# Optimization experiments

Hardware: AMD Instinct MI355X
Metric: run time of the kernel (lower is better)

## Reference

```python
import jax, jax.numpy as jnp
import numpy as np

D_EMB = 256
SCALE = 0.02
B, T = 4, 4096
EPS = 1e-5


def layer_norm(x, w, b):
    m = jnp.mean(x, axis=-1, keepdims=True)
    v = jnp.mean((x - m) ** 2, axis=-1, keepdims=True)
    return (x - m) * jax.lax.rsqrt(v + EPS) * w + b


def setup_inputs() -> dict:
    key = jax.random.key(0)
    ks = jax.random.split(key, 4)
    x = jax.random.normal(ks[0], (B, T, D_EMB), dtype=jnp.float32)
    qkv = jax.random.normal(ks[1], (3, D_EMB, D_EMB), dtype=jnp.float32) * SCALE
    # nn.Linear(D, 2D, bias=False): weight shape (2D, D), applied as x @ W.T
    w1 = jax.random.normal(ks[2], (2 * D_EMB, D_EMB), dtype=jnp.float32) * (1.0 / np.sqrt(D_EMB))
    w2 = jax.random.normal(ks[3], (D_EMB, 2 * D_EMB), dtype=jnp.float32) * (1.0 / np.sqrt(2 * D_EMB))
    ones = jnp.ones((D_EMB,), dtype=jnp.float32)
    zeros = jnp.zeros((D_EMB,), dtype=jnp.float32)
    return {
        "x": x, "qkv": qkv,
        "ln_q_w": ones, "ln_q_b": zeros,
        "ln_k_w": ones, "ln_k_b": zeros,
        "ln_attn_w": ones, "ln_attn_b": zeros,
        "w1": w1, "w2": w2,
        "ln_ff_w": ones, "ln_ff_b": zeros,
    }


def reference(x, qkv, ln_q_w, ln_q_b, ln_k_w, ln_k_b, ln_attn_w, ln_attn_b, w1, w2, ln_ff_w, ln_ff_b):
    # QKV projections: [3, B, T, D]
    y = jnp.einsum('btd,ndD->nbtD', x, qkv)
    q, k, v = y[0], y[1], y[2]
    q = layer_norm(q, ln_q_w, ln_q_b)
    k = layer_norm(k, ln_k_w, ln_k_b)
    # full (non-causal) single-head attention, scale by sqrt(D_EMB)
    scores = jnp.einsum('btd,bsd->bts', q, k) / jnp.sqrt(jnp.float32(D_EMB))
    attn = jax.nn.softmax(scores, axis=-1)
    y = jnp.einsum('bts,bsd->btd', attn, v)
    y = layer_norm(y, ln_attn_w, ln_attn_b)
    x = 0.7 * (x + y)
    # FFN with dual leaky_relu
    y = jax.nn.leaky_relu(x @ w1.T, negative_slope=0.2)
    y = jax.nn.leaky_relu(y @ w2.T, negative_slope=0.2)
    y = layer_norm(y, ln_ff_w, ln_ff_b)
    return 0.7 * (x + y)
```

## Files before the change

kernel.cpp:

```cpp
#include <hip/hip_runtime.h>

#define BSZ   4
#define TSEQ  4096
#define DEMB  256
#define NTOK  (BSZ * TSEQ)
#define HID   512
#define SPLITS 4
#define KEYS_PER_SPLIT (TSEQ / SPLITS)
#define TK 32
#define KIMG_STRIDE 8704
#define VIMG_STRIDE 10240

using bf16x8 = __attribute__((ext_vector_type(8))) short;
using f32x16 = __attribute__((ext_vector_type(16))) float;

static __device__ __forceinline__ unsigned short f2bf(float f) {
  union { float f; unsigned u; } v; v.f = f;
  unsigned r = v.u + 0x7FFF + ((v.u >> 16) & 1);
  return (unsigned short)(r >> 16);
}
static __device__ __forceinline__ float bf2f(unsigned short u) {
  union { unsigned u; float f; } v; v.u = ((unsigned)u) << 16;
  return v.f;
}

static __device__ __forceinline__ void async16(void* lds, const void* gp) {
  __builtin_amdgcn_global_load_lds(
      (const __attribute__((address_space(1))) unsigned int*)gp,
      (__attribute__((address_space(3))) unsigned int*)lds, 16, 0, 0);
}

__global__ __launch_bounds__(256) void prep_kernel(
    const float* __restrict__ qkv, const float* __restrict__ w1,
    const float* __restrict__ w2, unsigned short* __restrict__ qkvT,
    unsigned short* __restrict__ w1b, unsigned short* __restrict__ w2b)
{
  const int tid = threadIdx.x;
  if (blockIdx.y < 3) {
    if (blockIdx.x >= 16) return;
    __shared__ float Ts[64][65];
    const int z  = blockIdx.y;
    const int k0 = (blockIdx.x >> 2) * 64;
    const int j0 = (blockIdx.x & 3) * 64;
    const float* src = qkv + (size_t)z * DEMB * DEMB + (size_t)k0 * DEMB + j0;
#pragma unroll
    for (int p = 0; p < 4; ++p) {
      int idx = p * 256 + tid;
      int r = idx >> 4, g = idx & 15;
      float4 v = *(const float4*)(src + (size_t)r * DEMB + g * 4);
      Ts[r][g * 4 + 0] = v.x; Ts[r][g * 4 + 1] = v.y;
      Ts[r][g * 4 + 2] = v.z; Ts[r][g * 4 + 3] = v.w;
    }
    __syncthreads();
    unsigned short* dst = qkvT + (size_t)z * DEMB * DEMB + (size_t)j0 * DEMB + k0;
#pragma unroll
    for (int p = 0; p < 4; ++p) {
      int idx = p * 256 + tid;
      int r = idx >> 4, g = idx & 15;
      ushort4 o;
      o.x = f2bf(Ts[g * 4 + 0][r]); o.y = f2bf(Ts[g * 4 + 1][r]);
      o.z = f2bf(Ts[g * 4 + 2][r]); o.w = f2bf(Ts[g * 4 + 3][r]);
      *(ushort4*)(dst + (size_t)r * DEMB + g * 4) = o;
    }
  } else {
    const float* s = (blockIdx.y == 3) ? w1 : w2;
    unsigned short* d = (blockIdx.y == 3) ? w1b : w2b;
    const int i = blockIdx.x * 256 + tid;
    float4 v = ((const float4*)s)[i];
    ushort4 o;
    o.x = f2bf(v.x); o.y = f2bf(v.y); o.z = f2bf(v.z); o.w = f2bf(v.w);
    ((ushort4*)d)[i] = o;
  }
}

template <int ACT, int MODE, int AF32>
__global__ __launch_bounds__(256, 3) void gemm_bf16_kernel(
    const void* __restrict__ Av, const unsigned short* __restrict__ Bt,
    float* __restrict__ Cf, unsigned short* __restrict__ C0,
    unsigned short* __restrict__ C1, unsigned short* __restrict__ C2,
    int M, int N, int K)
{
  __shared__ __align__(16) unsigned short As[128 * 72];
  __shared__ __align__(16) unsigned short Bs[128 * 72];

  const int tid = threadIdx.x;
  const int w   = tid >> 6;
  const int wm  = w >> 1, wn = w & 1;
  const int l   = tid & 63;
  const int lm  = l & 31;
  const int lh  = l >> 5;

  const int m0    = blockIdx.x * 128;
  const int nbase = blockIdx.y * 128;

  f32x16 acc00, acc01, acc10, acc11;
#pragma unroll
  for (int r = 0; r < 16; ++r) { acc00[r] = 0.f; acc01[r] = 0.f; acc10[r] = 0.f; acc11[r] = 0.f; }

  const int lr = tid >> 3;
  const int lc = (tid & 7) * 8;
  const int fr = tid >> 4;
  const int fc = (tid & 15) * 4;

  const unsigned short* Ab = (const unsigned short*)Av;
  const float* Af = (const float*)Av;

  bf16x8 arb[4], brb[4];
  float4 arf[8];

#pragma unroll
  for (int i = 0; i < (AF32 ? 8 : 4); ++i) {
    if (AF32) arf[i] = *(const float4*)(Af + (size_t)(m0 + i * 16 + fr) * K + fc);
    else      arb[i] = *(const bf16x8*)(Ab + (size_t)(m0 + i * 32 + lr) * K + lc);
  }
#pragma unroll
  for (int i = 0; i < 4; ++i)
    brb[i] = *(const bf16x8*)(Bt + (size_t)(nbase + i * 32 + lr) * K + lc);

  for (int k0 = 0; k0 < K; k0 += 64) {
    __syncthreads();
    if (AF32) {
#pragma unroll
      for (int i = 0; i < 8; ++i) {
        ushort4 u;
        u.x = f2bf(arf[i].x); u.y = f2bf(arf[i].y);
        u.z = f2bf(arf[i].z); u.w = f2bf(arf[i].w);
        *(ushort4*)&As[(i * 16 + fr) * 72 + fc] = u;
      }
    } else {
#pragma unroll
      for (int i = 0; i < 4; ++i) *(bf16x8*)&As[(i * 32 + lr) * 72 + lc] = arb[i];
    }
#pragma unroll
    for (int i = 0; i < 4; ++i) *(bf16x8*)&Bs[(i * 32 + lr) * 72 + lc] = brb[i];
    __syncthreads();

    if (k0 + 64 < K) {
      const int kn = k0 + 64;
#pragma unroll
      for (int i = 0; i < (AF32 ? 8 : 4); ++i) {
        if (AF32) arf[i] = *(const float4*)(Af + (size_t)(m0 + i * 16 + fr) * K + kn + fc);
        else      arb[i] = *(const bf16x8*)(Ab + (size_t)(m0 + i * 32 + lr) * K + kn + lc);
      }
#pragma unroll
      for (int i = 0; i < 4; ++i)
        brb[i] = *(const bf16x8*)(Bt + (size_t)(nbase + i * 32 + lr) * K + kn + lc);
    }

#pragma unroll
    for (int ks = 0; ks < 4; ++ks) {
      bf16x8 a0 = *(const bf16x8*)&As[(wm * 64 + lm)      * 72 + ks * 16 + lh * 8];
      bf16x8 a1 = *(const bf16x8*)&As[(wm * 64 + 32 + lm) * 72 + ks * 16 + lh * 8];
      bf16x8 b0 = *(const bf16x8*)&Bs[(wn * 64 + lm)      * 72 + ks * 16 + lh * 8];
      bf16x8 b1 = *(const bf16x8*)&Bs[(wn * 64 + 32 + lm) * 72 + ks * 16 + lh * 8];
      acc00 = __builtin_amdgcn_mfma_f32_32x32x16_bf16(a0, b0, acc00, 0, 0, 0);
      acc01 = __builtin_amdgcn_mfma_f32_32x32x16_bf16(a0, b1, acc01, 0, 0, 0);
      acc10 = __builtin_amdgcn_mfma_f32_32x32x16_bf16(a1, b0, acc10, 0, 0, 0);
      acc11 = __builtin_amdgcn_mfma_f32_32x32x16_bf16(a1, b1, acc11, 0, 0, 0);
    }
  }

  unsigned short* Cb = C0;
  int col0, ldc;
  if (MODE == 2) {
    const int sel = blockIdx.y >> 1;
    Cb = (sel == 0) ? C0 : (sel == 1 ? C1 : C2);
    col0 = (blockIdx.y & 1) * 128;
    ldc = DEMB;
  } else {
    col0 = nbase;
    ldc = N;
  }
  const f32x16* accs[4] = { &acc00, &acc01, &acc10, &acc11 };
#pragma unroll
  for (int am = 0; am < 2; ++am)
#pragma unroll
    for (int bn = 0; bn < 2; ++bn) {
      const f32x16& a = *accs[am * 2 + bn];
#pragma unroll
      for (int r = 0; r < 16; ++r) {
        const int m = m0 + wm * 64 + am * 32 + (r & 3) + 8 * (r >> 2) + 4 * lh;
        const int n = col0 + wn * 64 + bn * 32 + lm;
        float v = a[r];
        if (ACT == 1) v = v > 0.f ? v : 0.2f * v;
        if (MODE == 0) Cf[(size_t)m * ldc + n] = v;
        else           Cb[(size_t)m * ldc + n] = f2bf(v);
      }
    }
}

__global__ __launch_bounds__(256) void ln_qk_kernel(
    const unsigned short* __restrict__ Qraw, const unsigned short* __restrict__ Kraw,
    const float* __restrict__ qw, const float* __restrict__ qb,
    const float* __restrict__ kw, const float* __restrict__ kb,
    unsigned short* __restrict__ Qbn, unsigned short* __restrict__ Kimg)
{
  const int isK = blockIdx.y;
  const unsigned short* X = isK ? Kraw : Qraw;
  const float* w = isK ? kw : qw;
  const float* b = isK ? kb : qb;
  const int lane = threadIdx.x & 63;
  const size_t row = (size_t)blockIdx.x * 4 + (threadIdx.x >> 6);
  ushort4 u = *(const ushort4*)&X[row * DEMB + lane * 4];
  float x0 = bf2f(u.x), x1 = bf2f(u.y), x2 = bf2f(u.z), x3 = bf2f(u.w);
  float s  = x0 + x1 + x2 + x3;
  float sq = x0 * x0 + x1 * x1 + x2 * x2 + x3 * x3;
#pragma unroll
  for (int o = 32; o > 0; o >>= 1) { s += __shfl_down(s, o); sq += __shfl_down(sq, o); }
  s = __shfl(s, 0); sq = __shfl(sq, 0);
  const float m  = s * (1.f / DEMB);
  const float rs = rsqrtf(sq * (1.f / DEMB) - m * m + 1e-5f);
  const float4 wv = *(const float4*)&w[lane * 4];
  const float4 bv = *(const float4*)&b[lane * 4];
  ushort4 o;
  o.x = f2bf((x0 - m) * rs * wv.x + bv.x);
  o.y = f2bf((x1 - m) * rs * wv.y + bv.y);
  o.z = f2bf((x2 - m) * rs * wv.z + bv.z);
  o.w = f2bf((x3 - m) * rs * wv.w + bv.w);
  if (!isK) {
    *(ushort4*)&Qbn[row * DEMB + lane * 4] = o;
  } else {
    const int bb = (int)(row >> 12);
    const int t  = (int)(row & 4095);
    *(ushort4*)&Kimg[(size_t)(bb * 128 + (t >> 5)) * KIMG_STRIDE + (t & 31) * 264 + lane * 4] = o;
  }
}

__global__ __launch_bounds__(256) void ln_res_kernel(
    const float* __restrict__ Y, const float* __restrict__ Xin,
    const float* __restrict__ w, const float* __restrict__ b,
    float* __restrict__ Out)
{
  const int lane = threadIdx.x & 63;
  const size_t row = (size_t)blockIdx.x * 4 + (threadIdx.x >> 6);
  float4 y = *(const float4*)&Y[row * DEMB + lane * 4];
  float s  = y.x + y.y + y.z + y.w;
  float sq = y.x * y.x + y.y * y.y + y.z * y.z + y.w * y.w;
#pragma unroll
  for (int o = 32; o > 0; o >>= 1) { s += __shfl_down(s, o); sq += __shfl_down(sq, o); }
  s = __shfl(s, 0); sq = __shfl(sq, 0);
  const float m  = s * (1.f / DEMB);
  const float rs = rsqrtf(sq * (1.f / DEMB) - m * m + 1e-5f);
  const float4 wv = *(const float4*)&w[lane * 4];
  const float4 bv = *(const float4*)&b[lane * 4];
  const float4 xi = *(const float4*)&Xin[row * DEMB + lane * 4];
  float4 o;
  o.x = 0.7f * (xi.x + (y.x - m) * rs * wv.x + bv.x);
  o.y = 0.7f * (xi.y + (y.y - m) * rs * wv.y + bv.y);
  o.z = 0.7f * (xi.z + (y.z - m) * rs * wv.z + bv.z);
  o.w = 0.7f * (xi.w + (y.w - m) * rs * wv.w + bv.w);
  *(float4*)&Out[row * DEMB + lane * 4] = o;
}

__global__ __launch_bounds__(256) void vtrans_img_kernel(
    const unsigned short* __restrict__ Vraw, unsigned short* __restrict__ Vimg)
{
  __shared__ float Ts[64][65];
  const int tid = threadIdx.x;
  const int t0 = blockIdx.x * 64;
  const int d0 = blockIdx.y * 64;
  const int b  = blockIdx.z;
  const unsigned short* src = Vraw + ((size_t)b * TSEQ + t0) * DEMB + d0;
#pragma unroll
  for (int p = 0; p < 4; ++p) {
    int idx = p * 256 + tid;
    int r = idx >> 4, g = idx & 15;
    ushort4 u = *(const ushort4*)(src + (size_t)r * DEMB + g * 4);
    Ts[r][g * 4 + 0] = bf2f(u.x); Ts[r][g * 4 + 1] = bf2f(u.y);
    Ts[r][g * 4 + 2] = bf2f(u.z); Ts[r][g * 4 + 3] = bf2f(u.w);
  }
  __syncthreads();
#pragma unroll
  for (int p = 0; p < 4; ++p) {
    int idx = p * 256 + tid;
    int r = idx >> 4, g = idx & 15;
    const int t  = t0 + g * 4;
    const int kt = t >> 5, toff = t & 31;
    ushort4 o;
    o.x = f2bf(Ts[g * 4 + 0][r]); o.y = f2bf(Ts[g * 4 + 1][r]);
    o.z = f2bf(Ts[g * 4 + 2][r]); o.w = f2bf(Ts[g * 4 + 3][r]);
    *(ushort4*)(Vimg + (size_t)(b * 128 + kt) * VIMG_STRIDE + (d0 + r) * 40 + toff) = o;
  }
}

__global__ __launch_bounds__(512) void attn_split_kernel(
    const unsigned short* __restrict__ Qb, const unsigned short* __restrict__ Kimg,
    const unsigned short* __restrict__ Vimg, unsigned short* __restrict__ Opart,
    float* __restrict__ lpart)
{
  __shared__ __align__(16) unsigned short Ks[2][KIMG_STRIDE];
  __shared__ __align__(16) unsigned short Vs[2][VIMG_STRIDE];
  __shared__ __align__(16) unsigned short Pb[8 * 32 * 40];

  const int tid = threadIdx.x;
  const int w   = tid >> 6;
  const int l   = tid & 63;
  const int lm  = l & 31;
  const int lh  = l >> 5;

  const int lin = blockIdx.x;
  const int xcd = lin & 7;
  const int idx = lin >> 3;
  const int b     = xcd >> 1;
  const int split = (xcd & 1) * 2 + (idx & 1);
  const int q0    = (idx >> 1) * 256;

  const unsigned short* Qbase  = Qb + (size_t)b * TSEQ * DEMB;
  const unsigned short* Ktiles = Kimg + (size_t)(b * 128 + split * 32) * KIMG_STRIDE;
  const unsigned short* Vtiles = Vimg + (size_t)(b * 128 + split * 32) * VIMG_STRIDE;

  bf16x8 qf[16];
  {
    const unsigned short* qrow = Qbase + (size_t)(q0 + w * 32 + lm) * DEMB + lh * 8;
#pragma unroll
    for (int ks = 0; ks < 16; ++ks) qf[ks] = *(const bf16x8*)(qrow + ks * 16);
  }

  f32x16 o[8];
  float lsum[16];
#pragma unroll
  for (int t = 0; t < 8; ++t)
#pragma unroll
    for (int r = 0; r < 16; ++r) o[t][r] = 0.f;
#pragma unroll
  for (int r = 0; r < 16; ++r) lsum[r] = 0.f;

  unsigned short* Pw = &Pb[w * 32 * 40];

#pragma unroll
  for (int i = 0; i < 3; ++i) {
    const int c = w + 8 * i;
    if (c < 17) async16(&Ks[0][c * 512], Ktiles + c * 512 + l * 8);
  }
#pragma unroll
  for (int i = 0; i < 3; ++i) {
    const int c = w + 8 * i;
    if (c < 20) async16(&Vs[0][c * 512], Vtiles + c * 512 + l * 8);
  }

  for (int st = 0; st < KEYS_PER_SPLIT / TK; ++st) {
    const int p = st & 1;
    __syncthreads();

    if (st + 1 < KEYS_PER_SPLIT / TK) {
      const unsigned short* kn = Ktiles + (size_t)(st + 1) * KIMG_STRIDE;
      const unsigned short* vn = Vtiles + (size_t)(st + 1) * VIMG_STRIDE;
#pragma unroll
      for (int i = 0; i < 3; ++i) {
        const int c = w + 8 * i;
        if (c < 17) async16(&Ks[1 - p][c * 512], kn + c * 512 + l * 8);
      }
#pragma unroll
      for (int i = 0; i < 3; ++i) {
        const int c = w + 8 * i;
        if (c < 20) async16(&Vs[1 - p][c * 512], vn + c * 512 + l * 8);
      }
    }

    f32x16 sa, sb;
#pragma unroll
    for (int r = 0; r < 16; ++r) { sa[r] = 0.f; sb[r] = 0.f; }
#pragma unroll
    for (int ks = 0; ks < 8; ++ks) {
      bf16x8 kfa = *(const bf16x8*)&Ks[p][lm * 264 + (2 * ks)     * 16 + lh * 8];
      bf16x8 kfb = *(const bf16x8*)&Ks[p][lm * 264 + (2 * ks + 1) * 16 + lh * 8];
      sa = __builtin_amdgcn_mfma_f32_32x32x16_bf16(qf[2 * ks],     kfa, sa, 0, 0, 0);
      sb = __builtin_amdgcn_mfma_f32_32x32x16_bf16(qf[2 * ks + 1], kfb, sb, 0, 0, 0);
    }

#pragma unroll
    for (int r = 0; r < 16; ++r) {
      const float pv = exp2f((sa[r] + sb[r]) * 0.09016844335f - 11.541560327f);
      lsum[r] += pv;
      const int row = (r & 3) + ((r >> 2) << 3) + (lh << 2);
      Pw[row * 40 + lm] = f2bf(pv);
    }

#pragma unroll
    for (int ks = 0; ks < 2; ++ks) {
      bf16x8 pf = *(const bf16x8*)&Pw[lm * 40 + ks * 16 + lh * 8];
#pragma unroll
      for (int t = 0; t < 8; ++t) {
        bf16x8 vf = *(const bf16x8*)&Vs[p][(t * 32 + lm) * 40 + ks * 16 + lh * 8];
        o[t] = __builtin_amdgcn_mfma_f32_32x32x16_bf16(pf, vf, o[t], 0, 0, 0);
      }
    }
  }

#pragma unroll
  for (int r = 0; r < 16; ++r) {
#pragma unroll
    for (int d = 1; d < 32; d <<= 1) lsum[r] += __shfl_xor(lsum[r], d, 64);
  }
  unsigned short* Ob =
      Opart + ((size_t)split * NTOK + (size_t)b * TSEQ + q0 + w * 32) * DEMB;
  float* lb = lpart + (size_t)split * NTOK + (size_t)b * TSEQ + q0 + w * 32;
#pragma unroll
  for (int r = 0; r < 16; ++r) {
    const int row = (r & 3) + ((r >> 2) << 3) + (lh << 2);
#pragma unroll
    for (int t = 0; t < 8; ++t)
      Ob[(size_t)row * DEMB + t * 32 + lm] = f2bf(o[t][r]);
    if (lm == 0) lb[row] = lsum[r];
  }
}

__global__ __launch_bounds__(256) void combine_lnres_kernel(
    const unsigned short* __restrict__ Opart, const float* __restrict__ lpart,
    const float* __restrict__ Xin, const float* __restrict__ w,
    const float* __restrict__ b, float* __restrict__ Out,
    unsigned short* __restrict__ Outb)
{
  const int lane = threadIdx.x & 63;
  const size_t row = (size_t)blockIdx.x * 4 + (threadIdx.x >> 6);
  float4 acc = make_float4(0.f, 0.f, 0.f, 0.f);
  float lt = 0.f;
#pragma unroll
  for (int p = 0; p < SPLITS; ++p) {
    const ushort4 u = *(const ushort4*)&Opart[((size_t)p * NTOK + row) * DEMB + lane * 4];
    acc.x += bf2f(u.x); acc.y += bf2f(u.y);
    acc.z += bf2f(u.z); acc.w += bf2f(u.w);
    lt += lpart[(size_t)p * NTOK + row];
  }
  const float inv = 1.f / lt;
  const float y0 = acc.x * inv, y1 = acc.y * inv, y2 = acc.z * inv, y3 = acc.w * inv;
  float s  = y0 + y1 + y2 + y3;
  float sq = y0 * y0 + y1 * y1 + y2 * y2 + y3 * y3;
#pragma unroll
  for (int o = 32; o > 0; o >>= 1) { s += __shfl_down(s, o); sq += __shfl_down(sq, o); }
  s = __shfl(s, 0); sq = __shfl(sq, 0);
  const float m  = s * (1.f / DEMB);
  const float rs = rsqrtf(sq * (1.f / DEMB) - m * m + 1e-5f);
  const float4 wv = *(const float4*)&w[lane * 4];
  const float4 bv = *(const float4*)&b[lane * 4];
  const float4 xi = *(const float4*)&Xin[row * DEMB + lane * 4];
  float4 o;
  o.x = 0.7f * (xi.x + (y0 - m) * rs * wv.x + bv.x);
  o.y = 0.7f * (xi.y + (y1 - m) * rs * wv.y + bv.y);
  o.z = 0.7f * (xi.z + (y2 - m) * rs * wv.z + bv.z);
  o.w = 0.7f * (xi.w + (y3 - m) * rs * wv.w + bv.w);
  *(float4*)&Out[row * DEMB + lane * 4] = o;
  ushort4 ob;
  ob.x = f2bf(o.x); ob.y = f2bf(o.y); ob.z = f2bf(o.z); ob.w = f2bf(o.w);
  *(ushort4*)&Outb[row * DEMB + lane * 4] = ob;
}

extern "C" void kernel_launch(void* const* d_in, const int* in_sizes, int n_in,
                              void* d_out, int out_size, void* d_ws, size_t ws_size,
                              hipStream_t stream)
{
  (void)in_sizes; (void)n_in; (void)out_size; (void)ws_size;
  const float* x    = (const float*)d_in[0];
  const float* qkv  = (const float*)d_in[1];
  const float* lnqw = (const float*)d_in[2];
  const float* lnqb = (const float*)d_in[3];
  const float* lnkw = (const float*)d_in[4];
  const float* lnkb = (const float*)d_in[5];
  const float* lnaw = (const float*)d_in[6];
  const float* lnab = (const float*)d_in[7];
  const float* w1   = (const float*)d_in[8];
  const float* w2   = (const float*)d_in[9];
  const float* lnfw = (const float*)d_in[10];
  const float* lnfb = (const float*)d_in[11];
  float* out = (float*)d_out;

  char* W = (char*)d_ws;
  const size_t MB = 1 << 20;
  unsigned short* Qraw  = (unsigned short*)(W + 8 * MB);
  unsigned short* Kraw  = (unsigned short*)(W + 16 * MB);
  unsigned short* Vraw  = (unsigned short*)(W + 24 * MB);
  unsigned short* Qbn   = (unsigned short*)(W + 32 * MB);
  unsigned short* Kimg  = (unsigned short*)(W + 40 * MB);
  unsigned short* Vimg  = (unsigned short*)(W + 49 * MB);
  unsigned short* Opart = (unsigned short*)(W + 0);
  float*          lpart = (float*)(W + 61 * MB);
  unsigned short* x1b   = (unsigned short*)(W + 32 * MB);
  unsigned short* H     = (unsigned short*)(W + 40 * MB);
  float*          Y2    = (float*)(W + 0);
  unsigned short* qkvT  = (unsigned short*)(W + 60 * MB);
  unsigned short* w1b   = (unsigned short*)(W + 60 * MB + 512 * 1024);
  unsigned short* w2b   = (unsigned short*)(W + 60 * MB + 768 * 1024);

  const dim3 blk(256);

  prep_kernel<<<dim3(128, 5), blk, 0, stream>>>(qkv, w1, w2, qkvT, w1b, w2b);

  gemm_bf16_kernel<0, 2, 1><<<dim3(NTOK / 128, 6), blk, 0, stream>>>(
      x, qkvT, nullptr, Qraw, Kraw, Vraw, NTOK, 3 * DEMB, DEMB);

  ln_qk_kernel<<<dim3(NTOK / 4, 2), blk, 0, stream>>>(
      Qraw, Kraw, lnqw, lnqb, lnkw, lnkb, Qbn, Kimg);
  vtrans_img_kernel<<<dim3(TSEQ / 64, DEMB / 64, BSZ), blk, 0, stream>>>(Vraw, Vimg);

  attn_split_kernel<<<dim3(256), dim3(512), 0, stream>>>(Qbn, Kimg, Vimg, Opart, lpart);
  combine_lnres_kernel<<<NTOK / 4, blk, 0, stream>>>(Opart, lpart, x, lnaw, lnab, out, x1b);

  gemm_bf16_kernel<1, 1, 0><<<dim3(NTOK / 128, HID / 128), blk, 0, stream>>>(
      x1b, w1b, nullptr, H, nullptr, nullptr, NTOK, HID, DEMB);
  gemm_bf16_kernel<1, 0, 0><<<dim3(NTOK / 128, DEMB / 128), blk, 0, stream>>>(
      H, w2b, Y2, nullptr, nullptr, nullptr, NTOK, DEMB, HID);

  ln_res_kernel<<<NTOK / 4, blk, 0, stream>>>(Y2, out, lnfw, lnfb, out);
}
```

Measured before the change: 255.0 us.

## Software-pipeline QK scores one tile ahead of PV and store FFN output in bf16

Restructures the attention key loop so the QK^T scores for tile st are computed after the PV product for tile st-1, with a peeled prologue and epilogue. V is triple-buffered in LDS so the previous tile stays resident while the next one is loaded. The intent is to overlap the exp/softmax and LDS P round-trip with MFMA work, and to merge the two score accumulators into one chain. Separately, the second FFN GEMM now writes bf16 instead of fp32, and the final layernorm reads bf16, halving that intermediate's traffic at some precision cost. The extra V buffer raises LDS use, which may lower occupancy.

```diff
diff --git a/kernel.cpp b/kernel.cpp
--- a/kernel.cpp
+++ b/kernel.cpp
@@ -8,6 +8,7 @@
 #define SPLITS 4
 #define KEYS_PER_SPLIT (TSEQ / SPLITS)
 #define TK 32
+#define NT (KEYS_PER_SPLIT / TK)
 #define KIMG_STRIDE 8704
 #define VIMG_STRIDE 10240
 
@@ -226,16 +227,17 @@
   }
 }
 
-__global__ __launch_bounds__(256) void ln_res_kernel(
-    const float* __restrict__ Y, const float* __restrict__ Xin,
+__global__ __launch_bounds__(256) void ln_res_bf16_kernel(
+    const unsigned short* __restrict__ Y, const float* __restrict__ Xin,
     const float* __restrict__ w, const float* __restrict__ b,
     float* __restrict__ Out)
 {
   const int lane = threadIdx.x & 63;
   const size_t row = (size_t)blockIdx.x * 4 + (threadIdx.x >> 6);
-  float4 y = *(const float4*)&Y[row * DEMB + lane * 4];
-  float s  = y.x + y.y + y.z + y.w;
-  float sq = y.x * y.x + y.y * y.y + y.z * y.z + y.w * y.w;
+  ushort4 u = *(const ushort4*)&Y[row * DEMB + lane * 4];
+  float y0 = bf2f(u.x), y1 = bf2f(u.y), y2 = bf2f(u.z), y3 = bf2f(u.w);
+  float s  = y0 + y1 + y2 + y3;
+  float sq = y0 * y0 + y1 * y1 + y2 * y2 + y3 * y3;
 #pragma unroll
   for (int o = 32; o > 0; o >>= 1) { s += __shfl_down(s, o); sq += __shfl_down(sq, o); }
   s = __shfl(s, 0); sq = __shfl(sq, 0);
@@ -245,10 +247,10 @@
   const float4 bv = *(const float4*)&b[lane * 4];
   const float4 xi = *(const float4*)&Xin[row * DEMB + lane * 4];
   float4 o;
-  o.x = 0.7f * (xi.x + (y.x - m) * rs * wv.x + bv.x);
-  o.y = 0.7f * (xi.y + (y.y - m) * rs * wv.y + bv.y);
-  o.z = 0.7f * (xi.z + (y.z - m) * rs * wv.z + bv.z);
-  o.w = 0.7f * (xi.w + (y.w - m) * rs * wv.w + bv.w);
+  o.x = 0.7f * (xi.x + (y0 - m) * rs * wv.x + bv.x);
+  o.y = 0.7f * (xi.y + (y1 - m) * rs * wv.y + bv.y);
+  o.z = 0.7f * (xi.z + (y2 - m) * rs * wv.z + bv.z);
+  o.w = 0.7f * (xi.w + (y3 - m) * rs * wv.w + bv.w);
   *(float4*)&Out[row * DEMB + lane * 4] = o;
 }
 
@@ -289,7 +291,7 @@
     float* __restrict__ lpart)
 {
   __shared__ __align__(16) unsigned short Ks[2][KIMG_STRIDE];
-  __shared__ __align__(16) unsigned short Vs[2][VIMG_STRIDE];
+  __shared__ __align__(16) unsigned short Vs[3][VIMG_STRIDE];
   __shared__ __align__(16) unsigned short Pb[8 * 32 * 40];
 
   const int tid = threadIdx.x;
@@ -317,7 +319,7 @@
   }
 
   f32x16 o[8];
-  float lsum[16];
+  float lsum[16], spv[16];
 #pragma unroll
   for (int t = 0; t < 8; ++t)
 #pragma unroll
@@ -338,50 +340,102 @@
     if (c < 20) async16(&Vs[0][c * 512], Vtiles + c * 512 + l * 8);
   }
 
-  for (int st = 0; st < KEYS_PER_SPLIT / TK; ++st) {
-    const int p = st & 1;
+  {
     __syncthreads();
-
-    if (st + 1 < KEYS_PER_SPLIT / TK) {
+#pragma unroll
+    for (int i = 0; i < 3; ++i) {
+      const int c = w + 8 * i;
+      if (c < 17) async16(&Ks[1][c * 512], Ktiles + (size_t)KIMG_STRIDE + c * 512 + l * 8);
+    }
+#pragma unroll
+    for (int i = 0; i < 3; ++i) {
+      const int c = w + 8 * i;
+      if (c < 20) async16(&Vs[1][c * 512], Vtiles + (size_t)VIMG_STRIDE + c * 512 + l * 8);
+    }
+    f32x16 s;
+#pragma unroll
+    for (int r = 0; r < 16; ++r) s[r] = 0.f;
+#pragma unroll
+    for (int ks = 0; ks < 16; ++ks) {
+      bf16x8 kf = *(const bf16x8*)&Ks[0][lm * 264 + ks * 16 + lh * 8];
+      s = __builtin_amdgcn_mfma_f32_32x32x16_bf16(qf[ks], kf, s, 0, 0, 0);
+    }
+#pragma unroll
+    for (int r = 0; r < 16; ++r) spv[r] = s[r];
+  }
+
+  int vprev = 0, vcur = 1, vnext = 2;
+
+  for (int st = 1; st < NT; ++st) {
+    __syncthreads();
+
+    if (st + 1 < NT) {
       const unsigned short* kn = Ktiles + (size_t)(st + 1) * KIMG_STRIDE;
       const unsigned short* vn = Vtiles + (size_t)(st + 1) * VIMG_STRIDE;
 #pragma unroll
       for (int i = 0; i < 3; ++i) {
         const int c = w + 8 * i;
-        if (c < 17) async16(&Ks[1 - p][c * 512], kn + c * 512 + l * 8);
+        if (c < 17) async16(&Ks[(st + 1) & 1][c * 512], kn + c * 512 + l * 8);
       }
 #pragma unroll
       for (int i = 0; i < 3; ++i) {
         const int c = w + 8 * i;
-        if (c < 20) async16(&Vs[1 - p][c * 512], vn + c * 512 + l * 8);
-      }
-    }
-
-    f32x16 sa, sb;
-#pragma unroll
-    for (int r = 0; r < 16; ++r) { sa[r] = 0.f; sb[r] = 0.f; }
-#pragma unroll
-    for (int ks = 0; ks < 8; ++ks) {
-      bf16x8 kfa = *(const bf16x8*)&Ks[p][lm * 264 + (2 * ks)     * 16 + lh * 8];
-      bf16x8 kfb = *(const bf16x8*)&Ks[p][lm * 264 + (2 * ks + 1) * 16 + lh * 8];
-      sa = __builtin_amdgcn_mfma_f32_32x32x16_bf16(qf[2 * ks],     kfa, sa, 0, 0, 0);
-      sb = __builtin_amdgcn_mfma_f32_32x32x16_bf16(qf[2 * ks + 1], kfb, sb, 0, 0, 0);
+        if (c < 20) async16(&Vs[vnext][c * 512], vn + c * 512 + l * 8);
+      }
     }
 
 #pragma unroll
     for (int r = 0; r < 16; ++r) {
-      const float pv = exp2f((sa[r] + sb[r]) * 0.09016844335f - 11.541560327f);
+      const float pv = exp2f(spv[r] * 0.09016844335f - 11.541560327f);
       lsum[r] += pv;
       const int row = (r & 3) + ((r >> 2) << 3) + (lh << 2);
       Pw[row * 40 + lm] = f2bf(pv);
     }
-
+    {
+      const unsigned short* Vp = &Vs[vprev][0];
+#pragma unroll
+      for (int ks = 0; ks < 2; ++ks) {
+        bf16x8 pf = *(const bf16x8*)&Pw[lm * 40 + ks * 16 + lh * 8];
+#pragma unroll
+        for (int t = 0; t < 8; ++t) {
+          bf16x8 vf = *(const bf16x8*)&Vp[(t * 32 + lm) * 40 + ks * 16 + lh * 8];
+          o[t] = __builtin_amdgcn_mfma_f32_32x32x16_bf16(pf, vf, o[t], 0, 0, 0);
+        }
+      }
+    }
+
+    {
+      f32x16 s;
+#pragma unroll
+      for (int r = 0; r < 16; ++r) s[r] = 0.f;
+      const unsigned short* Kp = &Ks[st & 1][0];
+#pragma unroll
+      for (int ks = 0; ks < 16; ++ks) {
+        bf16x8 kf = *(const bf16x8*)&Kp[lm * 264 + ks * 16 + lh * 8];
+        s = __builtin_amdgcn_mfma_f32_32x32x16_bf16(qf[ks], kf, s, 0, 0, 0);
+      }
+#pragma unroll
+      for (int r = 0; r < 16; ++r) spv[r] = s[r];
+    }
+
+    const int tmp = vprev; vprev = vcur; vcur = vnext; vnext = tmp;
+  }
+
+#pragma unroll
+  for (int r = 0; r < 16; ++r) {
+    const float pv = exp2f(spv[r] * 0.09016844335f - 11.541560327f);
+    lsum[r] += pv;
+    const int row = (r & 3) + ((r >> 2) << 3) + (lh << 2);
+    Pw[row * 40 + lm] = f2bf(pv);
+  }
+  {
+    const unsigned short* Vp = &Vs[vprev][0];
 #pragma unroll
     for (int ks = 0; ks < 2; ++ks) {
       bf16x8 pf = *(const bf16x8*)&Pw[lm * 40 + ks * 16 + lh * 8];
 #pragma unroll
       for (int t = 0; t < 8; ++t) {
-        bf16x8 vf = *(const bf16x8*)&Vs[p][(t * 32 + lm) * 40 + ks * 16 + lh * 8];
+        bf16x8 vf = *(const bf16x8*)&Vp[(t * 32 + lm) * 40 + ks * 16 + lh * 8];
         o[t] = __builtin_amdgcn_mfma_f32_32x32x16_bf16(pf, vf, o[t], 0, 0, 0);
       }
     }
@@ -476,7 +530,7 @@
   float*          lpart = (float*)(W + 61 * MB);
   unsigned short* x1b   = (unsigned short*)(W + 32 * MB);
   unsigned short* H     = (unsigned short*)(W + 40 * MB);
-  float*          Y2    = (float*)(W + 0);
+  unsigned short* Y2b   = (unsigned short*)(W + 0);
   unsigned short* qkvT  = (unsigned short*)(W + 60 * MB);
   unsigned short* w1b   = (unsigned short*)(W + 60 * MB + 512 * 1024);
   unsigned short* w2b   = (unsigned short*)(W + 60 * MB + 768 * 1024);
@@ -497,8 +551,8 @@
 
   gemm_bf16_kernel<1, 1, 0><<<dim3(NTOK / 128, HID / 128), blk, 0, stream>>>(
       x1b, w1b, nullptr, H, nullptr, nullptr, NTOK, HID, DEMB);
-  gemm_bf16_kernel<1, 0, 0><<<dim3(NTOK / 128, DEMB / 128), blk, 0, stream>>>(
-      H, w2b, Y2, nullptr, nullptr, nullptr, NTOK, DEMB, HID);
-
-  ln_res_kernel<<<NTOK / 4, blk, 0, stream>>>(Y2, out, lnfw, lnfb, out);
-}
+  gemm_bf16_kernel<1, 1, 0><<<dim3(NTOK / 128, DEMB / 128), blk, 0, stream>>>(
+      H, w2b, nullptr, Y2b, nullptr, nullptr, NTOK, DEMB, HID);
+
+  ln_res_bf16_kernel<<<NTOK / 4, blk, 0, stream>>>(Y2b, out, lnfw, lnfb, out);
+}
```

New measurement: 235.5 us. 1.08x faster.
